# Performance work log

Measured on AMD Instinct MI355X. Metric: run time of the kernel, lower is better.

Reference implementation:

```python
import jax, jax.numpy as jnp
import numpy as np

BN_EPS = 1e-5

def setup_inputs() -> dict:
    key = jax.random.key(0)
    ks = jax.random.split(key, 12)
    B = 32768
    x = jax.random.normal(ks[0], (B, 1, 28, 28), dtype=jnp.float32)
    conv_w = jax.random.normal(ks[1], (5, 1, 6, 6), dtype=jnp.float32) * 0.1
    conv_b = jax.random.normal(ks[2], (5,), dtype=jnp.float32) * 0.1
    bn2_gamma = jnp.ones((5,), jnp.float32) + jax.random.normal(ks[3], (5,), jnp.float32) * 0.05
    bn2_beta = jax.random.normal(ks[4], (5,), jnp.float32) * 0.05
    bn2_mean = jax.random.normal(ks[5], (5,), jnp.float32) * 0.1
    bn2_var = jax.random.uniform(ks[6], (5,), jnp.float32, 0.5, 1.5)
    fc_w = jax.random.normal(ks[7], (10, 125), dtype=jnp.float32) * 0.1
    fc_b = jax.random.normal(ks[8], (10,), dtype=jnp.float32) * 0.1
    bn1_gamma = jnp.ones((10,), jnp.float32) + jax.random.normal(ks[9], (10,), jnp.float32) * 0.05
    bn1_beta = jax.random.normal(ks[10], (10,), jnp.float32) * 0.05
    bn1_mean = jax.random.normal(ks[11], (10,), jnp.float32) * 0.1
    bn1_var = jnp.ones((10,), jnp.float32)
    return {"x": x, "conv_w": conv_w, "conv_b": conv_b,
            "bn2_gamma": bn2_gamma, "bn2_beta": bn2_beta, "bn2_mean": bn2_mean, "bn2_var": bn2_var,
            "fc_w": fc_w, "fc_b": fc_b,
            "bn1_gamma": bn1_gamma, "bn1_beta": bn1_beta, "bn1_mean": bn1_mean, "bn1_var": bn1_var}

def _sign(t):
    # torch Binarize = tensor.sign()
    return jnp.sign(t)

def reference(x, conv_w, conv_b, bn2_gamma, bn2_beta, bn2_mean, bn2_var,
              fc_w, fc_b, bn1_gamma, bn1_beta, bn1_mean, bn1_var):
    # BinarizeConv2d: binarize both input (C_in=1 != 3) and weight
    xb = _sign(x)
    wb = _sign(conv_w)
    y = jax.lax.conv_general_dilated(
        xb, wb, window_strides=(6, 6), padding=((2, 2), (2, 2)),
        dimension_numbers=("NCHW", "OIHW", "NCHW"))  # [B,5,5,5]
    y = y + conv_b[None, :, None, None]
    # BatchNorm2d (eval-mode running stats)
    y = (y - bn2_mean[None, :, None, None]) * (bn2_gamma / jnp.sqrt(bn2_var + BN_EPS))[None, :, None, None] + bn2_beta[None, :, None, None]
    # Hardtanh
    y = jnp.clip(y, -1.0, 1.0)
    # flatten to [B, 125]
    y = y.reshape(-1, 125)
    # BinarizeLinear: binarize input (125 != 784) and weight
    z = _sign(y) @ _sign(fc_w).T + fc_b
    # BatchNorm1d
    z = (z - bn1_mean) * (bn1_gamma / jnp.sqrt(bn1_var + BN_EPS)) + bn1_beta
    return jax.nn.log_softmax(z, axis=1)
```

## Files before the change

### kernel.cpp

```cpp
#include <hip/hip_runtime.h>
#include <cstdint>

#define BLK 256
#define SPB 8
#define XS_INTS (16 + SPB*240)


__global__ __launch_bounds__(BLK, 4)
void bnn_fused(const float* __restrict__ x,
               const float* __restrict__ conv_w,
               const float* __restrict__ conv_b,
               const float* __restrict__ bn2_g,
               const float* __restrict__ bn2_b,
               const float* __restrict__ bn2_m,
               const float* __restrict__ bn2_v,
               const float* __restrict__ fc_w,
               const float* __restrict__ fc_b,
               const float* __restrict__ bn1_g,
               const float* __restrict__ bn1_b,
               const float* __restrict__ bn1_m,
               const float* __restrict__ bn1_v,
               float* __restrict__ out)
{
    __shared__ int   xsi[XS_INTS];
    __shared__ int   ysi[SPB*32];
    __shared__ int   wmsk[64];
    __shared__ int   fmsk[320];
    __shared__ int   nnegI[8];
    __shared__ int   fnegI[16];
    __shared__ float zf[SPB*10];

    const int tid = threadIdx.x;
    const int blk = blockIdx.x;

    for (int i = tid; i < 16 + SPB*44; i += BLK) {
        int idx;
        if (i < 16) idx = i;
        else {
            int j = i - 16; int s = j / 44; int k = j - s*44;
            idx = 16 + s*240 + (k < 16 ? k : ((k - 16 + 2)*8 + 7));
        }
        xsi[idx] = 0;
    }
    for (int i = tid; i < SPB*32; i += BLK) ysi[i] = 0;

    for (int i = tid; i < 320; i += BLK) {
        int o = i >> 5, w = i & 31;
        uint32_t mm = 0;
        #pragma unroll
        for (int k = 0; k < 4; k++) {
            int kk = w*4 + k;
            if (kk < 125) mm |= (fc_w[o*125 + kk] < 0.f) ? (0xFFu << (8*k)) : 0u;
        }
        fmsk[i] = (int)mm;
    }
    if (tid < 30) {
        int c = tid / 6, kr = tid - c*6;
        const float* wp = conv_w + c*36 + kr*6;
        uint32_t m0 = 0, m1 = 0;
        #pragma unroll
        for (int k = 0; k < 4; k++) m0 |= (wp[k]   < 0.f) ? (0xFFu << (8*k)) : 0u;
        #pragma unroll
        for (int k = 0; k < 2; k++) m1 |= (wp[4+k] < 0.f) ? (0xFFu << (8*k)) : 0u;
        wmsk[tid*2 + 0] = (int)m0;
        wmsk[tid*2 + 1] = (int)m1;
    }
    if (tid >= 32 && tid < 37) {
        int c = tid - 32, cnt = 0;
        for (int k = 0; k < 36; k++) cnt += (conv_w[c*36 + k] < 0.f);
        nnegI[c] = cnt;
    }
    if (tid >= 64 && tid < 74) {
        int o = tid - 64, cnt = 0;
        for (int k = 0; k < 125; k++) cnt += (fc_w[o*125 + k] < 0.f);
        fnegI[o] = cnt;
    }
    {
        const float4* xg = (const float4*)x + (size_t)blk * (SPB*196);
        for (int i = tid; i < SPB*196; i += BLK) {
            float4 v = xg[i];
            int s = i / 196, rem = i - s*196;
            int r = rem / 7,  cq  = rem - r*7;
            int b0 = (v.x > 0.f) - (v.x < 0.f);
            int b1 = (v.y > 0.f) - (v.y < 0.f);
            int b2 = (v.z > 0.f) - (v.z < 0.f);
            int b3 = (v.w > 0.f) - (v.w < 0.f);
            int packed = (b0 & 0xFF) | ((b1 & 0xFF) << 8) | ((b2 & 0xFF) << 16) | (b3 << 24);
            xsi[16 + s*240 + (r+2)*8 + cq] = packed;
        }
    }
    __syncthreads();

    if (tid < 250) {
        const int c  = tid / 50;
        const int jb = tid - c*50;
        int m[12];
        #pragma unroll
        for (int i = 0; i < 12; i++) m[i] = wmsk[c*12 + i];
        const int   nneg  = nnegI[c];
        const float cb    = conv_b[c];
        const float mean  = bn2_m[c];
        const float scale = bn2_g[c] / sqrtf(bn2_v[c] + 1e-5f);
        const float beta  = bn2_b[c];
        #pragma unroll
        for (int t = 0; t < (SPB*25)/50; t++) {
            int j  = jb + 50*t;
            int s  = j / 25, pos = j - s*25;
            int oh = pos / 5, ow  = pos - oh*5;
            int boff = 64 + s*960 + oh*192 + ow*6 - 2;
            int wi = boff >> 2;
            int sh = (boff & 3) * 8;
            int acc = 0;
            #pragma unroll
            for (int kr = 0; kr < 6; kr++) {
                uint32_t w0 = (uint32_t)xsi[wi + kr*8];
                uint32_t w1 = (uint32_t)xsi[wi + kr*8 + 1];
                uint64_t vv = ((uint64_t)w1 << 32) | (uint64_t)w0;
                vv >>= sh;
                uint32_t e0 = (uint32_t)vv         ^ (uint32_t)m[kr*2 + 0];
                uint32_t e1 = (uint32_t)(vv >> 32) ^ (uint32_t)m[kr*2 + 1];
                acc += ((int)(e0 << 24)) >> 24;
                acc += ((int)(e0 << 16)) >> 24;
                acc += ((int)(e0 <<  8)) >> 24;
                acc += ((int)(e0      )) >> 24;
                acc += ((int)(e1 << 24)) >> 24;
                acc += ((int)(e1 << 16)) >> 24;
            }
            float conv = (float)(acc + nneg);
            float yv = ((conv + cb) - mean) * scale + beta;
            signed char sb = (signed char)((yv > 0.f) - (yv < 0.f));
            ((signed char*)ysi)[s*128 + c*25 + pos] = sb;
        }
    }
    __syncthreads();

    for (int item = tid; item < SPB*10; item += BLK) {
        int s = item / 10, o = item - s*10;
        int acc = 0;
        #pragma unroll
        for (int w = 0; w < 32; w++) {
            uint32_t tb = (uint32_t)ysi[s*32 + w] ^ (uint32_t)fmsk[o*32 + w];
            acc += ((int)(tb << 24)) >> 24;
            acc += ((int)(tb << 16)) >> 24;
            acc += ((int)(tb <<  8)) >> 24;
            acc += ((int)(tb      )) >> 24;
        }
        float z  = (float)(acc + fnegI[o]) + fc_b[o];
        float sc = bn1_g[o] / sqrtf(bn1_v[o] + 1e-5f);
        zf[item] = (z - bn1_m[o]) * sc + bn1_b[o];
    }
    __syncthreads();

    if (tid < SPB) {
        float v[10], mx = -1e30f;
        #pragma unroll
        for (int o = 0; o < 10; o++) { v[o] = zf[tid*10 + o]; mx = fmaxf(mx, v[o]); }
        float l = 0.f;
        #pragma unroll
        for (int o = 0; o < 10; o++) l += __expf(v[o] - mx);
        float lse = mx + __logf(l);
        #pragma unroll
        for (int o = 0; o < 10; o++) zf[tid*10 + o] = v[o] - lse;
    }
    __syncthreads();

    for (int i = tid; i < SPB*10; i += BLK)
        out[(size_t)blk * (SPB*10) + i] = zf[i];
}

extern "C" void kernel_launch(void* const* d_in, const int* in_sizes, int n_in,
                              void* d_out, int out_size, void* d_ws, size_t ws_size,
                              hipStream_t stream)
{
    const float* xp     = (const float*)d_in[0];
    const float* conv_w = (const float*)d_in[1];
    const float* conv_b = (const float*)d_in[2];
    const float* bn2_g  = (const float*)d_in[3];
    const float* bn2_b  = (const float*)d_in[4];
    const float* bn2_m  = (const float*)d_in[5];
    const float* bn2_v  = (const float*)d_in[6];
    const float* fc_w   = (const float*)d_in[7];
    const float* fc_b   = (const float*)d_in[8];
    const float* bn1_g  = (const float*)d_in[9];
    const float* bn1_b  = (const float*)d_in[10];
    const float* bn1_m  = (const float*)d_in[11];
    const float* bn1_v  = (const float*)d_in[12];
    float* outp = (float*)d_out;

    const int B = in_sizes[0] / 784;
    const int grid = B / SPB;
    bnn_fused<<<grid, BLK, 0, stream>>>(xp, conv_w, conv_b,
                                        bn2_g, bn2_b, bn2_m, bn2_v,
                                        fc_w, fc_b,
                                        bn1_g, bn1_b, bn1_m, bn1_v,
                                        outp);
}
```

Baseline: 203.0 us.

## Precompute weight masks in setup kernel, use sdot4, prefetch input, pad smem rows

```diff
diff --git a/kernel.cpp b/kernel.cpp
--- a/kernel.cpp
+++ b/kernel.cpp
@@ -3,169 +3,187 @@
 
 #define BLK 256
 #define SPB 8
-#define XS_INTS (16 + SPB*240)
-
+#define RS  9
+#define SS  (30*RS)
+#define HDR 16
+#define XS_INTS (HDR + SPB*SS)
+#define YS_W 33
+
+#if defined(__has_builtin)
+# if __has_builtin(__builtin_amdgcn_sdot4)
+#  define HAVE_SDOT4 1
+# endif
+#endif
+
+__device__ __forceinline__ int dot4i8(int a, int b, int c) {
+#ifdef HAVE_SDOT4
+    return __builtin_amdgcn_sdot4(a, b, c, false);
+#else
+    int r = c;
+    r += (((int)(a << 24)) >> 24) * (((int)(b << 24)) >> 24);
+    r += (((int)(a << 16)) >> 24) * (((int)(b << 16)) >> 24);
+    r += (((int)(a <<  8)) >> 24) * (((int)(b <<  8)) >> 24);
+    r += (a >> 24) * (b >> 24);
+    return r;
+#endif
+}
+
+__device__ __forceinline__ int pack_sign4(float4 v) {
+    int b0 = (v.x > 0.f) - (v.x < 0.f);
+    int b1 = (v.y > 0.f) - (v.y < 0.f);
+    int b2 = (v.z > 0.f) - (v.z < 0.f);
+    int b3 = (v.w > 0.f) - (v.w < 0.f);
+    return (b0 & 0xFF) | ((b1 & 0xFF) << 8) | ((b2 & 0xFF) << 16) | (b3 << 24);
+}
+
+__global__ void bnn_setup(const float* __restrict__ conv_w, const float* __restrict__ conv_b,
+                          const float* __restrict__ bn2_g, const float* __restrict__ bn2_b,
+                          const float* __restrict__ bn2_m, const float* __restrict__ bn2_v,
+                          const float* __restrict__ fc_w,  const float* __restrict__ fc_b,
+                          const float* __restrict__ bn1_g, const float* __restrict__ bn1_b,
+                          const float* __restrict__ bn1_m, const float* __restrict__ bn1_v,
+                          int* __restrict__ ws)
+{
+    const int tid = threadIdx.x;
+    if (tid < 30) {
+        int c = tid / 6, kr = tid - c * 6;
+        const float* wp = conv_w + c * 36 + kr * 6;
+        uint32_t a = 0, b = 0;
+        #pragma unroll
+        for (int k = 0; k < 4; k++) { int s = (wp[k]   > 0.f) - (wp[k]   < 0.f); a |= (uint32_t)(s & 0xFF) << (8 * k); }
+        #pragma unroll
+        for (int k = 0; k < 2; k++) { int s = (wp[4+k] > 0.f) - (wp[4+k] < 0.f); b |= (uint32_t)(s & 0xFF) << (8 * k); }
+        ws[tid] = (int)a;
+        ws[30 + tid] = (int)b;
+    }
+    for (int i = tid; i < 330; i += 64) {
+        int o = i / 33, w = i - o * 33;
+        uint32_t m = 0;
+        #pragma unroll
+        for (int k = 0; k < 4; k++) {
+            int kk = w * 4 + k;
+            if (kk < 125) { float f = fc_w[o * 125 + kk]; int s = (f > 0.f) - (f < 0.f); m |= (uint32_t)(s & 0xFF) << (8 * k); }
+        }
+        ws[60 + i] = (int)m;
+    }
+    if (tid < 5) {
+        float sc = bn2_g[tid] / sqrtf(bn2_v[tid] + 1e-5f);
+        ((float*)ws)[390 + tid] = sc;
+        ((float*)ws)[395 + tid] = (conv_b[tid] - bn2_m[tid]) * sc + bn2_b[tid];
+    }
+    if (tid >= 32 && tid < 42) {
+        int o = tid - 32;
+        float sc = bn1_g[o] / sqrtf(bn1_v[o] + 1e-5f);
+        ((float*)ws)[400 + o] = sc;
+        ((float*)ws)[410 + o] = (fc_b[o] - bn1_m[o]) * sc + bn1_b[o];
+    }
+}
 
 __global__ __launch_bounds__(BLK, 4)
-void bnn_fused(const float* __restrict__ x,
-               const float* __restrict__ conv_w,
-               const float* __restrict__ conv_b,
-               const float* __restrict__ bn2_g,
-               const float* __restrict__ bn2_b,
-               const float* __restrict__ bn2_m,
-               const float* __restrict__ bn2_v,
-               const float* __restrict__ fc_w,
-               const float* __restrict__ fc_b,
-               const float* __restrict__ bn1_g,
-               const float* __restrict__ bn1_b,
-               const float* __restrict__ bn1_m,
-               const float* __restrict__ bn1_v,
-               float* __restrict__ out)
+void bnn_main(const float* __restrict__ x, const int* __restrict__ ws,
+              float* __restrict__ out)
 {
     __shared__ int   xsi[XS_INTS];
-    __shared__ int   ysi[SPB*32];
-    __shared__ int   wmsk[64];
-    __shared__ int   fmsk[320];
-    __shared__ int   nnegI[8];
-    __shared__ int   fnegI[16];
-    __shared__ float zf[SPB*10];
+    __shared__ int   ysi[SPB * YS_W];
+    __shared__ int   wsS[420];
+    __shared__ float zf[SPB * 10];
 
     const int tid = threadIdx.x;
     const int blk = blockIdx.x;
 
-    for (int i = tid; i < 16 + SPB*44; i += BLK) {
+    const float4* xg = (const float4*)x + (size_t)blk * (SPB * 196);
+    float4 v[6]; float4 v6;
+    #pragma unroll
+    for (int k = 0; k < 6; k++) v[k] = xg[tid + k * BLK];
+    const bool has7 = tid < (SPB * 196 - 6 * BLK);
+    if (has7) v6 = xg[tid + 6 * BLK];
+
+    for (int i = tid; i < 420; i += BLK) wsS[i] = ws[i];
+
+    for (int i = tid; i < HDR + SPB * 74; i += BLK) {
         int idx;
-        if (i < 16) idx = i;
+        if (i < HDR) idx = i;
         else {
-            int j = i - 16; int s = j / 44; int k = j - s*44;
-            idx = 16 + s*240 + (k < 16 ? k : ((k - 16 + 2)*8 + 7));
+            int j = i - HDR, s = j / 74, k = j - s * 74;
+            idx = HDR + s * SS + (k < 18 ? k : (2 + (k - 18) / 2) * RS + 7 + ((k - 18) & 1));
         }
         xsi[idx] = 0;
     }
-    for (int i = tid; i < SPB*32; i += BLK) ysi[i] = 0;
-
-    for (int i = tid; i < 320; i += BLK) {
-        int o = i >> 5, w = i & 31;
-        uint32_t mm = 0;
-        #pragma unroll
-        for (int k = 0; k < 4; k++) {
-            int kk = w*4 + k;
-            if (kk < 125) mm |= (fc_w[o*125 + kk] < 0.f) ? (0xFFu << (8*k)) : 0u;
-        }
-        fmsk[i] = (int)mm;
-    }
-    if (tid < 30) {
-        int c = tid / 6, kr = tid - c*6;
-        const float* wp = conv_w + c*36 + kr*6;
-        uint32_t m0 = 0, m1 = 0;
-        #pragma unroll
-        for (int k = 0; k < 4; k++) m0 |= (wp[k]   < 0.f) ? (0xFFu << (8*k)) : 0u;
-        #pragma unroll
-        for (int k = 0; k < 2; k++) m1 |= (wp[4+k] < 0.f) ? (0xFFu << (8*k)) : 0u;
-        wmsk[tid*2 + 0] = (int)m0;
-        wmsk[tid*2 + 1] = (int)m1;
-    }
-    if (tid >= 32 && tid < 37) {
-        int c = tid - 32, cnt = 0;
-        for (int k = 0; k < 36; k++) cnt += (conv_w[c*36 + k] < 0.f);
-        nnegI[c] = cnt;
-    }
-    if (tid >= 64 && tid < 74) {
-        int o = tid - 64, cnt = 0;
-        for (int k = 0; k < 125; k++) cnt += (fc_w[o*125 + k] < 0.f);
-        fnegI[o] = cnt;
-    }
-    {
-        const float4* xg = (const float4*)x + (size_t)blk * (SPB*196);
-        for (int i = tid; i < SPB*196; i += BLK) {
-            float4 v = xg[i];
-            int s = i / 196, rem = i - s*196;
-            int r = rem / 7,  cq  = rem - r*7;
-            int b0 = (v.x > 0.f) - (v.x < 0.f);
-            int b1 = (v.y > 0.f) - (v.y < 0.f);
-            int b2 = (v.z > 0.f) - (v.z < 0.f);
-            int b3 = (v.w > 0.f) - (v.w < 0.f);
-            int packed = (b0 & 0xFF) | ((b1 & 0xFF) << 8) | ((b2 & 0xFF) << 16) | (b3 << 24);
-            xsi[16 + s*240 + (r+2)*8 + cq] = packed;
-        }
+    for (int i = tid; i < SPB * YS_W; i += BLK) ysi[i] = 0;
+
+    #pragma unroll
+    for (int k = 0; k < 6; k++) {
+        int idx = tid + k * BLK;
+        int s = idx / 196, rem = idx - s * 196;
+        int r = rem / 7,   cq  = rem - r * 7;
+        xsi[HDR + s * SS + (r + 2) * RS + cq] = pack_sign4(v[k]);
+    }
+    if (has7) {
+        int idx = tid + 6 * BLK;
+        int s = idx / 196, rem = idx - s * 196;
+        int r = rem / 7,   cq  = rem - r * 7;
+        xsi[HDR + s * SS + (r + 2) * RS + cq] = pack_sign4(v6);
     }
     __syncthreads();
 
     if (tid < 250) {
         const int c  = tid / 50;
-        const int jb = tid - c*50;
-        int m[12];
-        #pragma unroll
-        for (int i = 0; i < 12; i++) m[i] = wmsk[c*12 + i];
-        const int   nneg  = nnegI[c];
-        const float cb    = conv_b[c];
-        const float mean  = bn2_m[c];
-        const float scale = bn2_g[c] / sqrtf(bn2_v[c] + 1e-5f);
-        const float beta  = bn2_b[c];
-        #pragma unroll
-        for (int t = 0; t < (SPB*25)/50; t++) {
-            int j  = jb + 50*t;
-            int s  = j / 25, pos = j - s*25;
-            int oh = pos / 5, ow  = pos - oh*5;
-            int boff = 64 + s*960 + oh*192 + ow*6 - 2;
+        const int jb = tid - c * 50;
+        int w0r[6], w1r[6];
+        #pragma unroll
+        for (int kr = 0; kr < 6; kr++) { w0r[kr] = wsS[c * 6 + kr]; w1r[kr] = wsS[30 + c * 6 + kr]; }
+        const float sc = __int_as_float(wsS[390 + c]);
+        const float bi = __int_as_float(wsS[395 + c]);
+        #pragma unroll
+        for (int t = 0; t < (SPB * 25) / 50; t++) {
+            int j  = jb + 50 * t;
+            int s  = j / 25, pos = j - s * 25;
+            int oh = pos / 5, ow  = pos - oh * 5;
+            int boff = 64 + s * (SS * 4) + oh * (6 * RS * 4) + ow * 6 - 2;
             int wi = boff >> 2;
             int sh = (boff & 3) * 8;
             int acc = 0;
             #pragma unroll
             for (int kr = 0; kr < 6; kr++) {
-                uint32_t w0 = (uint32_t)xsi[wi + kr*8];
-                uint32_t w1 = (uint32_t)xsi[wi + kr*8 + 1];
-                uint64_t vv = ((uint64_t)w1 << 32) | (uint64_t)w0;
+                uint32_t a0 = (uint32_t)xsi[wi + kr * RS];
+                uint32_t a1 = (uint32_t)xsi[wi + kr * RS + 1];
+                uint64_t vv = (((uint64_t)a1) << 32) | a0;
                 vv >>= sh;
-                uint32_t e0 = (uint32_t)vv         ^ (uint32_t)m[kr*2 + 0];
-                uint32_t e1 = (uint32_t)(vv >> 32) ^ (uint32_t)m[kr*2 + 1];
-                acc += ((int)(e0 << 24)) >> 24;
-                acc += ((int)(e0 << 16)) >> 24;
-                acc += ((int)(e0 <<  8)) >> 24;
-                acc += ((int)(e0      )) >> 24;
-                acc += ((int)(e1 << 24)) >> 24;
-                acc += ((int)(e1 << 16)) >> 24;
+                acc = dot4i8((int)(uint32_t)vv,         w0r[kr], acc);
+                acc = dot4i8((int)(uint32_t)(vv >> 32), w1r[kr], acc);
             }
-            float conv = (float)(acc + nneg);
-            float yv = ((conv + cb) - mean) * scale + beta;
-            signed char sb = (signed char)((yv > 0.f) - (yv < 0.f));
-            ((signed char*)ysi)[s*128 + c*25 + pos] = sb;
+            float yv = (float)acc * sc + bi;
+            ((signed char*)ysi)[s * (YS_W * 4) + c * 25 + pos] =
+                (signed char)((yv > 0.f) - (yv < 0.f));
         }
     }
     __syncthreads();
 
-    for (int item = tid; item < SPB*10; item += BLK) {
-        int s = item / 10, o = item - s*10;
+    if (tid < SPB * 10) {
+        int s = tid / 10, o = tid - s * 10;
         int acc = 0;
         #pragma unroll
-        for (int w = 0; w < 32; w++) {
-            uint32_t tb = (uint32_t)ysi[s*32 + w] ^ (uint32_t)fmsk[o*32 + w];
-            acc += ((int)(tb << 24)) >> 24;
-            acc += ((int)(tb << 16)) >> 24;
-            acc += ((int)(tb <<  8)) >> 24;
-            acc += ((int)(tb      )) >> 24;
-        }
-        float z  = (float)(acc + fnegI[o]) + fc_b[o];
-        float sc = bn1_g[o] / sqrtf(bn1_v[o] + 1e-5f);
-        zf[item] = (z - bn1_m[o]) * sc + bn1_b[o];
+        for (int w = 0; w < 32; w++)
+            acc = dot4i8(ysi[s * YS_W + w], wsS[60 + o * 33 + w], acc);
+        zf[tid] = (float)acc * __int_as_float(wsS[400 + o]) + __int_as_float(wsS[410 + o]);
     }
     __syncthreads();
 
     if (tid < SPB) {
-        float v[10], mx = -1e30f;
-        #pragma unroll
-        for (int o = 0; o < 10; o++) { v[o] = zf[tid*10 + o]; mx = fmaxf(mx, v[o]); }
+        float vv[10], mx = -1e30f;
+        #pragma unroll
+        for (int o = 0; o < 10; o++) { vv[o] = zf[tid * 10 + o]; mx = fmaxf(mx, vv[o]); }
         float l = 0.f;
         #pragma unroll
-        for (int o = 0; o < 10; o++) l += __expf(v[o] - mx);
+        for (int o = 0; o < 10; o++) l += __expf(vv[o] - mx);
         float lse = mx + __logf(l);
         #pragma unroll
-        for (int o = 0; o < 10; o++) zf[tid*10 + o] = v[o] - lse;
-    }
-    __syncthreads();
-
-    for (int i = tid; i < SPB*10; i += BLK)
-        out[(size_t)blk * (SPB*10) + i] = zf[i];
+        for (int o = 0; o < 10; o++) zf[tid * 10 + o] = vv[o] - lse;
+    }
+    __syncthreads();
+
+    for (int i = tid; i < SPB * 10; i += BLK)
+        out[(size_t)blk * (SPB * 10) + i] = zf[i];
 }
 
 extern "C" void kernel_launch(void* const* d_in, const int* in_sizes, int n_in,
@@ -186,12 +204,12 @@
     const float* bn1_m  = (const float*)d_in[11];
     const float* bn1_v  = (const float*)d_in[12];
     float* outp = (float*)d_out;
+    int*   ws   = (int*)d_ws;
 
     const int B = in_sizes[0] / 784;
     const int grid = B / SPB;
-    bnn_fused<<<grid, BLK, 0, stream>>>(xp, conv_w, conv_b,
-                                        bn2_g, bn2_b, bn2_m, bn2_v,
-                                        fc_w, fc_b,
-                                        bn1_g, bn1_b, bn1_m, bn1_v,
-                                        outp);
-}
+
+    bnn_setup<<<1, 64, 0, stream>>>(conv_w, conv_b, bn2_g, bn2_b, bn2_m, bn2_v,
+                                    fc_w, fc_b, bn1_g, bn1_b, bn1_m, bn1_v, ws);
+    bnn_main<<<grid, BLK, 0, stream>>>(xp, ws, outp);
+}
```

Result: faster. 179.8 us (-11.4%).
